# Kernel tuning notes

Measured on AMD Instinct MI355X. Metric: run time of the kernel, lower is better.

Reference implementation:

```python
import jax, jax.numpy as jnp
import numpy as np

EPS = 1e-6

def _ste(x, xq):
    return x + jax.lax.stop_gradient(xq - x)

def rmsnorm(x, w):
    return x * jax.lax.rsqrt(jnp.mean(x * x, axis=-1, keepdims=True) + EPS) * w

def act_quant(x):
    # per-token absmax int8 quantization (BitNet b1.58)
    s = 127.0 / jnp.clip(jnp.max(jnp.abs(x), axis=-1, keepdims=True), 1e-5)
    return _ste(x, jnp.clip(jnp.round(x * s), -128, 127) / s)

def w_quant(w):
    # per-tensor mean-absmax ternary quantization
    s = 1.0 / jnp.clip(jnp.mean(jnp.abs(w)), 1e-5)
    return _ste(w, jnp.clip(jnp.round(w * s), -1, 1) / s)

def bitlinear(x, w):
    return act_quant(x) @ w_quant(w).T

def snake_beta(x, log_a, log_b):
    a = jnp.exp(log_a)
    b = jnp.exp(log_b)
    s = jnp.sin(a * x)
    return x + (1.0 / (b + 1e-9)) * s * s

def ffn(x, nw, w1, la, lb, w2):
    h = bitlinear(rmsnorm(x, nw), w1)
    return bitlinear(snake_beta(h, la, lb), w2)

def mha(x, nw, ipw, ipb, opw, opb, num_heads):
    B, T, D = x.shape
    hd = D // num_heads
    xn = rmsnorm(x, nw)
    qkv = xn @ ipw.T + ipb  # [B,T,3D]
    q, k, v = jnp.split(qkv, 3, axis=-1)
    def heads(t):
        return t.reshape(B, T, num_heads, hd).transpose(0, 2, 1, 3)  # [B,H,T,hd]
    q, k, v = heads(q), heads(k), heads(v)
    scores = jnp.einsum('bhqd,bhkd->bhqk', q, k) / jnp.sqrt(jnp.asarray(hd, x.dtype))
    attn = jax.nn.softmax(scores, axis=-1)
    o = jnp.einsum('bhqk,bhkd->bhqd', attn, v)
    o = o.transpose(0, 2, 1, 3).reshape(B, T, D)
    return o @ opw.T + opb

def conv_branch(x, nw, pw1, dw, dwb, bg, bb, bm, bv, la, lb, pw2, K):
    B, T, D = x.shape
    h = rmsnorm(x, nw)
    h = bitlinear(h, pw1)  # [B,T,2D] (1x1 BitConv1d)
    a, g = jnp.split(h, 2, axis=-1)
    h = a * jax.nn.sigmoid(g)  # GLU over channels
    hc = h.transpose(0, 2, 1)  # [B,D,T]
    hc = jax.lax.conv_general_dilated(
        hc, dw, window_strides=(1,), padding=[(K // 2, K // 2)],
        feature_group_count=D, dimension_numbers=('NCH', 'OIH', 'NCH'))
    hc = hc + dwb[None, :, None]
    hc = (hc - bm[None, :, None]) * jax.lax.rsqrt(bv[None, :, None] + 1e-5) * bg[None, :, None] + bb[None, :, None]
    h = hc.transpose(0, 2, 1)  # [B,T,D]
    h = snake_beta(h, la, lb)
    return bitlinear(h, pw2)

def setup_inputs() -> dict:
    key = jax.random.key(0)
    B, T, D, H, K = 4, 2048, 512, 8, 31
    ks = jax.random.split(key, 16)
    n = lambda k, s: (jax.random.normal(k, s, jnp.float32) * 0.02)
    d = {
        'x': jax.random.normal(ks[0], (B, T, D), jnp.float32),
        'ff1_norm_w': jnp.ones((D,), jnp.float32),
        'ff1_w1': n(ks[1], (4 * D, D)), 'ff1_a': jnp.zeros((4 * D,), jnp.float32),
        'ff1_b': jnp.zeros((4 * D,), jnp.float32), 'ff1_w2': n(ks[2], (D, 4 * D)),
        'attn_norm_w': jnp.ones((D,), jnp.float32),
        'in_proj_w': n(ks[3], (3 * D, D)), 'in_proj_b': jnp.zeros((3 * D,), jnp.float32),
        'out_proj_w': n(ks[4], (D, D)), 'out_proj_b': jnp.zeros((D,), jnp.float32),
        'conv_norm_w': jnp.ones((D,), jnp.float32),
        'pw1_w': n(ks[5], (2 * D, D)),
        'dw_w': n(ks[6], (D, 1, K)), 'dw_b': jnp.zeros((D,), jnp.float32),
        'bn_g': jnp.ones((D,), jnp.float32), 'bn_b': jnp.zeros((D,), jnp.float32),
        'bn_m': jnp.zeros((D,), jnp.float32), 'bn_v': jnp.ones((D,), jnp.float32),
        'snake_a': jnp.zeros((D,), jnp.float32), 'snake_b': jnp.zeros((D,), jnp.float32),
        'pw2_w': n(ks[7], (D, D)),
        'ff2_norm_w': jnp.ones((D,), jnp.float32),
        'ff2_w1': n(ks[8], (4 * D, D)), 'ff2_a': jnp.zeros((4 * D,), jnp.float32),
        'ff2_b': jnp.zeros((4 * D,), jnp.float32), 'ff2_w2': n(ks[9], (D, 4 * D)),
        'final_norm_w': jnp.ones((D,), jnp.float32),
    }
    return d

def reference(x, ff1_norm_w, ff1_w1, ff1_a, ff1_b, ff1_w2, attn_norm_w, in_proj_w, in_proj_b, out_proj_w, out_proj_b, conv_norm_w, pw1_w, dw_w, dw_b, bn_g, bn_b, bn_m, bn_v, snake_a, snake_b, pw2_w, ff2_norm_w, ff2_w1, ff2_a, ff2_b, ff2_w2, final_norm_w):
    H, K = 8, 31
    x = x + 0.5 * ffn(x, ff1_norm_w, ff1_w1, ff1_a, ff1_b, ff1_w2)
    x = x + mha(x, attn_norm_w, in_proj_w, in_proj_b, out_proj_w, out_proj_b, H)
    x = x + conv_branch(x, conv_norm_w, pw1_w, dw_w, dw_b, bn_g, bn_b, bn_m, bn_v, snake_a, snake_b, pw2_w, K)
    x = x + 0.5 * ffn(x, ff2_norm_w, ff2_w1, ff2_a, ff2_b, ff2_w2)
    return rmsnorm(x, final_norm_w)
```

## Files before the change

kernel.cpp:

```cpp
#include <hip/hip_runtime.h>
#include <math.h>


typedef int   v4i __attribute__((ext_vector_type(4)));
typedef float v4f __attribute__((ext_vector_type(4)));
typedef float v16f __attribute__((ext_vector_type(16)));
typedef short v8s __attribute__((ext_vector_type(8)));
typedef unsigned short u16;

#define GLOAD_LDS(g, l) __builtin_amdgcn_global_load_lds( \
    (const __attribute__((address_space(1))) void*)(g),   \
    (__attribute__((address_space(3))) void*)(l), 16, 0, 0)

__device__ __forceinline__ float blk_sum256(float v, float* sm) {
#pragma unroll
  for (int m = 32; m; m >>= 1) v += __shfl_xor(v, m);
  int w = threadIdx.x >> 6;
  __syncthreads();
  if ((threadIdx.x & 63) == 0) sm[w] = v;
  __syncthreads();
  return sm[0] + sm[1] + sm[2] + sm[3];
}

__device__ __forceinline__ u16 f2bf(float f) {
  union { float f; unsigned u; } x;
  x.f = f;
  unsigned r = x.u + 0x7fffu + ((x.u >> 16) & 1u);
  return (u16)(r >> 16);
}

__device__ __forceinline__ float bf2f(u16 u) {
  union { unsigned u; float f; } x;
  x.u = ((unsigned)u) << 16;
  return x.f;
}

__device__ __forceinline__ void xcd_tiles(int& tx, int& ty) {
  int nx = gridDim.x;
  int flat = blockIdx.y * nx + blockIdx.x;
  int nwg = nx * gridDim.y;
  int cpx = nwg >> 3;
  int swz = (flat & 7) * cpx + (flat >> 3);
  ty = swz / nx;
  tx = swz - ty * nx;
}

__global__ __launch_bounds__(256) void wabs_stage1(
    const float* __restrict__ w0, const float* __restrict__ w1,
    const float* __restrict__ w2, const float* __restrict__ w3,
    const float* __restrict__ w4, const float* __restrict__ w5,
    float* __restrict__ part) {
  __shared__ float sm[4];
  const float* ws[6] = {w0, w1, w2, w3, w4, w5};
  const int ns[6] = {1048576, 1048576, 524288, 262144, 1048576, 1048576};
  int widx = blockIdx.x >> 6;
  int chunk = blockIdx.x & 63;
  const float* w = ws[widx];
  int n = ns[widx];
  float s = 0.f;
  for (int i = chunk * 256 + threadIdx.x; i < n; i += 64 * 256) s += fabsf(w[i]);
  s = blk_sum256(s, sm);
  if (threadIdx.x == 0) part[widx * 64 + chunk] = s;
}

__global__ __launch_bounds__(256) void wquant_all(
    const float* __restrict__ w0, const float* __restrict__ w1,
    const float* __restrict__ w2, const float* __restrict__ w3,
    const float* __restrict__ w4, const float* __restrict__ w5,
    const float* __restrict__ part, float* __restrict__ scales,
    signed char* __restrict__ out) {
  const float* ws[6] = {w0, w1, w2, w3, w4, w5};
  const int ns[6] = {1048576, 1048576, 524288, 262144, 1048576, 1048576};
  const int offs[6] = {0, 1048576, 2097152, 2621440, 2883584, 3932160};
  int widx = blockIdx.y;
  const float* w = ws[widx];
  int n = ns[widx];
  signed char* o = out + offs[widx];
  float ssum = 0.f;
#pragma unroll 8
  for (int i = 0; i < 64; ++i) ssum += part[widx * 64 + i];
  float wsc = fmaxf(ssum / (float)n, 1e-5f);
  if (blockIdx.x == 0 && threadIdx.x == 0) scales[widx] = wsc;
  float s = 1.0f / wsc;
  for (int i = blockIdx.x * 256 + threadIdx.x; i < n; i += 128 * 256)
    o[i] = (signed char)(int)fminf(fmaxf(rintf(w[i] * s), -1.f), 1.f);
}

__global__ __launch_bounds__(256) void wcvt_tabs(
    const float* __restrict__ ip, const float* __restrict__ op, u16* __restrict__ wb,
    const float* __restrict__ a1, const float* __restrict__ b1,
    const float* __restrict__ a2, const float* __restrict__ b2,
    float* __restrict__ tabs, const float* __restrict__ x, u16* __restrict__ xbf) {
  int bid = blockIdx.x;
  if (bid < 4096) {
    int i = bid * 256 + threadIdx.x;
    if (i < 786432) wb[i] = f2bf(ip[i]);
    else wb[i] = f2bf(op[i - 786432]);
  } else if (bid < 4104) {
    int i = (bid - 4096) * 256 + threadIdx.x;
    if (i < 2048) {
      tabs[i] = __expf(a1[i]);
      tabs[2048 + i] = 1.0f / (__expf(b1[i]) + 1e-9f);
      tabs[4096 + i] = __expf(a2[i]);
      tabs[6144 + i] = 1.0f / (__expf(b2[i]) + 1e-9f);
    }
  } else {
    size_t i = ((size_t)(bid - 4104) * 256 + threadIdx.x) * 8;
    float4 f0 = *(const float4*)(x + i);
    float4 f1 = *(const float4*)(x + i + 4);
    v8s o;
    o[0] = (short)f2bf(f0.x); o[1] = (short)f2bf(f0.y);
    o[2] = (short)f2bf(f0.z); o[3] = (short)f2bf(f0.w);
    o[4] = (short)f2bf(f1.x); o[5] = (short)f2bf(f1.y);
    o[6] = (short)f2bf(f1.z); o[7] = (short)f2bf(f1.w);
    *(v8s*)(xbf + i) = o;
  }
}

__global__ __launch_bounds__(256) void rmsnorm_wave(
    const u16* __restrict__ x, const float* __restrict__ w, int mode,
    float* __restrict__ outf, signed char* __restrict__ out8,
    u16* __restrict__ outb, float* __restrict__ dq) {
  const int tid = threadIdx.x;
  const int lane = tid & 63, wv = tid >> 6;
  const int row = blockIdx.x * 4 + wv;
  const int c0 = lane * 8;
  v8s xv = *(const v8s*)(x + (size_t)row * 512 + c0);
  float v[8];
  float ss = 0.f;
#pragma unroll
  for (int j = 0; j < 8; ++j) {
    v[j] = bf2f((u16)xv[j]);
    ss = fmaf(v[j], v[j], ss);
  }
#pragma unroll
  for (int m = 1; m < 64; m <<= 1) ss += __shfl_xor(ss, m);
  float sc = 1.0f / sqrtf(ss * (1.0f / 512.0f) + 1e-6f);
  float4 w0 = *(const float4*)(w + c0);
  float4 w1 = *(const float4*)(w + c0 + 4);
  float wv8[8] = {w0.x, w0.y, w0.z, w0.w, w1.x, w1.y, w1.z, w1.w};
  float y[8];
#pragma unroll
  for (int j = 0; j < 8; ++j) y[j] = v[j] * sc * wv8[j];
  if (mode == 0) {
    float* o = outf + (size_t)row * 512 + c0;
    *(float4*)o = make_float4(y[0], y[1], y[2], y[3]);
    *(float4*)(o + 4) = make_float4(y[4], y[5], y[6], y[7]);
  } else if (mode == 1) {
    float am = 0.f;
#pragma unroll
    for (int j = 0; j < 8; ++j) am = fmaxf(am, fabsf(y[j]));
#pragma unroll
    for (int m = 1; m < 64; m <<= 1) am = fmaxf(am, __shfl_xor(am, m));
    float amc = fmaxf(am, 1e-5f);
    float s = 127.0f / amc;
    unsigned long long pkt = 0;
#pragma unroll
    for (int j = 0; j < 8; ++j) {
      int q = (int)rintf(y[j] * s);
      pkt |= ((unsigned long long)(unsigned char)(signed char)q) << (8 * j);
    }
    *(unsigned long long*)(out8 + (size_t)row * 512 + c0) = pkt;
    if (lane == 0) dq[row] = amc * (1.0f / 127.0f);
  } else {
    v8s o;
#pragma unroll
    for (int j = 0; j < 8; ++j) o[j] = (short)f2bf(y[j]);
    *(v8s*)(outb + (size_t)row * 512 + c0) = o;
  }
}

__global__ __launch_bounds__(256) void snake_wave(
    const u16* __restrict__ h, const float* __restrict__ ta, const float* __restrict__ tb,
    signed char* __restrict__ out, float* __restrict__ dq) {
  const int tid = threadIdx.x;
  const int lane = tid & 63, wv = tid >> 6;
  const int row = blockIdx.x * 4 + wv;
  const u16* hr = h + (size_t)row * 2048;
  float vals[32];
  float am = 0.f;
#pragma unroll
  for (int g = 0; g < 4; ++g) {
    int c0 = g * 512 + lane * 8;
    v8s hv = *(const v8s*)(hr + c0);
    float4 ta0 = *(const float4*)(ta + c0);
    float4 ta1 = *(const float4*)(ta + c0 + 4);
    float4 tb0 = *(const float4*)(tb + c0);
    float4 tb1 = *(const float4*)(tb + c0 + 4);
    float sa[8] = {ta0.x, ta0.y, ta0.z, ta0.w, ta1.x, ta1.y, ta1.z, ta1.w};
    float sib[8] = {tb0.x, tb0.y, tb0.z, tb0.w, tb1.x, tb1.y, tb1.z, tb1.w};
#pragma unroll
    for (int j = 0; j < 8; ++j) {
      float v = bf2f((u16)hv[j]);
      float s = __sinf(sa[j] * v);
      v += s * s * sib[j];
      vals[g * 8 + j] = v;
      am = fmaxf(am, fabsf(v));
    }
  }
#pragma unroll
  for (int m = 1; m < 64; m <<= 1) am = fmaxf(am, __shfl_xor(am, m));
  float amc = fmaxf(am, 1e-5f);
  float s = 127.0f / amc;
#pragma unroll
  for (int g = 0; g < 4; ++g) {
    unsigned long long pkt = 0;
#pragma unroll
    for (int j = 0; j < 8; ++j) {
      int q = (int)rintf(vals[g * 8 + j] * s);
      pkt |= ((unsigned long long)(unsigned char)(signed char)q) << (8 * j);
    }
    *(unsigned long long*)(out + (size_t)row * 2048 + g * 512 + lane * 8) = pkt;
  }
  if (lane == 0) dq[row] = amc * (1.0f / 127.0f);
}

__global__ __launch_bounds__(256) void rowquant_wave(
    const u16* __restrict__ in, signed char* __restrict__ out, float* __restrict__ dq) {
  const int tid = threadIdx.x;
  const int lane = tid & 63, wv = tid >> 6;
  const int row = blockIdx.x * 4 + wv;
  const int c0 = lane * 8;
  v8s xv = *(const v8s*)(in + (size_t)row * 512 + c0);
  float v[8];
  float am = 0.f;
#pragma unroll
  for (int j = 0; j < 8; ++j) {
    v[j] = bf2f((u16)xv[j]);
    am = fmaxf(am, fabsf(v[j]));
  }
#pragma unroll
  for (int m = 1; m < 64; m <<= 1) am = fmaxf(am, __shfl_xor(am, m));
  float amc = fmaxf(am, 1e-5f);
  float s = 127.0f / amc;
  unsigned long long pkt = 0;
#pragma unroll
  for (int j = 0; j < 8; ++j) {
    int q = (int)rintf(v[j] * s);
    pkt |= ((unsigned long long)(unsigned char)(signed char)q) << (8 * j);
  }
  *(unsigned long long*)(out + (size_t)row * 512 + c0) = pkt;
  if (lane == 0) dq[row] = amc * (1.0f / 127.0f);
}

template <int BN, int OM>
__global__ __launch_bounds__(256) void gemm_i8_t(
    const signed char* __restrict__ A, const signed char* __restrict__ B,
    const float* __restrict__ wsp, const float* __restrict__ adq,
    const u16* __restrict__ resid, float rscale,
    u16* __restrict__ outb, int N, int K) {
  constexpr int JF = BN / 32;
  __shared__ signed char As[16384];
  __shared__ signed char Bs[BN * 128];
  const int tid = threadIdx.x;
  int txc, tyc;
  xcd_tiles(txc, tyc);
  const int m0 = tyc << 7;
  const int n0 = txc * BN;
  const int lane = tid & 63;
  const int wv = tid >> 6;
  const int wr = (wv >> 1) << 6, wc = (wv & 1) * (16 * JF);
  const int r15 = lane & 15, khi = lane >> 4;
  const int srow = tid >> 3;
  const int sslot = (tid & 7) ^ (srow & 7);
  const signed char* Ag = A + (size_t)(m0 + srow) * K + sslot * 16;
  const signed char* Bg = B + (size_t)(n0 + srow) * K + sslot * 16;
  const size_t row32 = (size_t)32 * K;

  int aoff[4][2], boff[JF][2];
#pragma unroll
  for (int i = 0; i < 4; ++i) {
    int r = wr + i * 16 + r15;
#pragma unroll
    for (int s = 0; s < 2; ++s)
      aoff[i][s] = r * 128 + (((s << 2) + khi) ^ (r & 7)) * 16;
  }
#pragma unroll
  for (int j = 0; j < JF; ++j) {
    int c = wc + j * 16 + r15;
#pragma unroll
    for (int s = 0; s < 2; ++s)
      boff[j][s] = c * 128 + (((s << 2) + khi) ^ (c & 7)) * 16;
  }
  v4i acc[4][JF] = {};
  for (int k0 = 0; k0 < K; k0 += 128) {
    __syncthreads();
#pragma unroll
    for (int c = 0; c < 4; ++c)
      GLOAD_LDS(Ag + c * row32 + k0, As + c * 4096 + tid * 16);
#pragma unroll
    for (int c = 0; c < BN / 32; ++c)
      GLOAD_LDS(Bg + c * row32 + k0, Bs + c * 4096 + tid * 16);
    __syncthreads();
    v4i a[4][2], b[JF][2];
#pragma unroll
    for (int i = 0; i < 4; ++i) {
      a[i][0] = *(const v4i*)(As + aoff[i][0]);
      a[i][1] = *(const v4i*)(As + aoff[i][1]);
    }
#pragma unroll
    for (int j = 0; j < JF; ++j) {
      b[j][0] = *(const v4i*)(Bs + boff[j][0]);
      b[j][1] = *(const v4i*)(Bs + boff[j][1]);
    }
#pragma unroll
    for (int i = 0; i < 4; ++i)
#pragma unroll
      for (int j = 0; j < JF; ++j) {
        acc[i][j] = __builtin_amdgcn_mfma_i32_16x16x64_i8(a[i][0], b[j][0], acc[i][j], 0, 0, 0);
        acc[i][j] = __builtin_amdgcn_mfma_i32_16x16x64_i8(a[i][1], b[j][1], acc[i][j], 0, 0, 0);
      }
  }
  const float wsc = *wsp;
#pragma unroll
  for (int i = 0; i < 4; ++i) {
    int rb = m0 + wr + i * 16 + (khi << 2);
    float dqv[4];
#pragma unroll
    for (int rr = 0; rr < 4; ++rr) dqv[rr] = adq[rb + rr] * wsc;
#pragma unroll
    for (int j = 0; j < JF; ++j) {
      int col = n0 + wc + j * 16 + r15;
#pragma unroll
      for (int rr = 0; rr < 4; ++rr) {
        size_t idx = (size_t)(rb + rr) * N + col;
        float v = (float)acc[i][j][rr] * dqv[rr];
        if constexpr (OM == 0) outb[idx] = f2bf(v);
        else outb[idx] = f2bf(fmaf(rscale, v, bf2f(resid[idx])));
      }
    }
  }
}

template <int BN, int OM>
__global__ __launch_bounds__(256) void gemm_bf16_t(
    const u16* __restrict__ A, const u16* __restrict__ B,
    const float* __restrict__ bias, const u16* __restrict__ resid,
    u16* __restrict__ outb, int N, int K) {
  constexpr int JF = BN / 32;
  __shared__ signed char As[8192];
  __shared__ signed char Bs[BN * 64];
  const int tid = threadIdx.x;
  int txc, tyc;
  xcd_tiles(txc, tyc);
  const int m0 = tyc << 7;
  const int n0 = txc * BN;
  const int lane = tid & 63;
  const int wv = tid >> 6;
  const int wr = (wv >> 1) << 6, wc = (wv & 1) * (16 * JF);
  const int r15 = lane & 15, khi = lane >> 4;
  const int srow = tid >> 2;
  const int sslot = (tid & 3) ^ ((srow >> 1) & 3);
  const int K2 = K * 2;
  const signed char* Ag = (const signed char*)A + (size_t)(m0 + srow) * K2 + sslot * 16;
  const signed char* Bg = (const signed char*)B + (size_t)(n0 + srow) * K2 + sslot * 16;
  const size_t half = (size_t)64 * K2;

  int aoff[4], boff[JF];
#pragma unroll
  for (int i = 0; i < 4; ++i) {
    int r = wr + i * 16 + r15;
    aoff[i] = r * 64 + ((khi ^ ((r >> 1) & 3)) << 4);
  }
#pragma unroll
  for (int j = 0; j < JF; ++j) {
    int c = wc + j * 16 + r15;
    boff[j] = c * 64 + ((khi ^ ((c >> 1) & 3)) << 4);
  }
  v4f acc[4][JF] = {};
  for (int kb = 0; kb < K2; kb += 64) {
    __syncthreads();
    GLOAD_LDS(Ag + kb, As + tid * 16);
    GLOAD_LDS(Ag + half + kb, As + 4096 + tid * 16);
    GLOAD_LDS(Bg + kb, Bs + tid * 16);
    if constexpr (BN == 128) GLOAD_LDS(Bg + half + kb, Bs + 4096 + tid * 16);
    __syncthreads();
    v8s a[4], b[JF];
#pragma unroll
    for (int i = 0; i < 4; ++i) a[i] = *(const v8s*)(As + aoff[i]);
#pragma unroll
    for (int j = 0; j < JF; ++j) b[j] = *(const v8s*)(Bs + boff[j]);
#pragma unroll
    for (int i = 0; i < 4; ++i)
#pragma unroll
      for (int j = 0; j < JF; ++j)
        acc[i][j] = __builtin_amdgcn_mfma_f32_16x16x32_bf16(a[i], b[j], acc[i][j], 0, 0, 0);
  }
#pragma unroll
  for (int i = 0; i < 4; ++i) {
    int rb = m0 + wr + i * 16 + (khi << 2);
#pragma unroll
    for (int j = 0; j < JF; ++j) {
      int col = n0 + wc + j * 16 + r15;
      float bv = bias[col];
#pragma unroll
      for (int rr = 0; rr < 4; ++rr) {
        size_t idx = (size_t)(rb + rr) * N + col;
        float v = acc[i][j][rr] + bv;
        if constexpr (OM == 0) outb[idx] = f2bf(v);
        else outb[idx] = f2bf(bf2f(resid[idx]) + v);
      }
    }
  }
}

__global__ __launch_bounds__(256) void kvqpack(
    const u16* __restrict__ qkv, u16* __restrict__ kvqp) {
  __shared__ u16 Lv[32 * 72];
  const int tid = threadIdx.x;
  const int tile = blockIdx.x;
  const int bh = blockIdx.y;
  const int b = bh >> 3, h = bh & 7;
  u16* outb = kvqp + ((size_t)(bh * 64 + tile)) * 6144;
  const int lane = tid & 63, f = tid >> 6;
  const int l31 = lane & 31, hi = lane >> 5;

  {
    int r = tid >> 3, c = (tid & 7) << 3;
    const u16* src = qkv + (size_t)(b * 2048 + tile * 32 + r) * 1536 + 1024 + h * 64 + c;
    *(v8s*)(&Lv[r * 72 + c]) = *(const v8s*)src;
  }
  {
    const u16* src = qkv + (size_t)(b * 2048 + tile * 32 + l31) * 1536 + h * 64 + f * 16 + hi * 8;
    *(v8s*)(outb + (size_t)(8 + f) * 512 + lane * 8) = *(const v8s*)src;
  }
  {
    const u16* src = qkv + (size_t)(b * 2048 + tile * 32 + l31) * 1536 + 512 + h * 64 + f * 16 + hi * 8;
    *(v8s*)(outb + (size_t)f * 512 + lane * 8) = *(const v8s*)src;
  }
  __syncthreads();
  {
    int d = ((f >> 1) << 5) + l31;
    int tbase = ((f & 1) << 4) + hi * 8;
    v8s v;
#pragma unroll
    for (int j = 0; j < 8; ++j) v[j] = (short)Lv[(tbase + j) * 72 + d];
    *(v8s*)(outb + (size_t)(4 + f) * 512 + lane * 8) = v;
  }
}

__global__ __launch_bounds__(256) void attn32(
    const u16* __restrict__ kvqp, u16* __restrict__ opart, float* __restrict__ ml) {
  __shared__ u16 KV[2][4096];
  const int tid = threadIdx.x;
  const int lane = tid & 63;
  const int wv = tid >> 6;
  const int l31 = lane & 31;
  const int hi = lane >> 5;
  const int bh = blockIdx.y;
  const int z = blockIdx.z;
  const int b = bh >> 3, h = bh & 7;
  const int qt = blockIdx.x * 4 + wv;
  const int q0 = qt << 5;
  const float C = 0.18033688011112042f;

  v8s qf[4];
  {
    const u16* qb = kvqp + ((size_t)(bh * 64 + qt)) * 6144 + lane * 8;
#pragma unroll
    for (int ks = 0; ks < 4; ++ks) qf[ks] = *(const v8s*)(qb + (8 + ks) * 512);
  }
  v16f o0 = {}, o1 = {};
  float m_run = -INFINITY, l_run = 0.f;

  const u16* tb = kvqp + ((size_t)(bh * 64 + z * 16)) * 6144;

  GLOAD_LDS(tb + tid * 8, &KV[0][tid * 8]);
  GLOAD_LDS(tb + 2048 + tid * 8, &KV[0][2048 + tid * 8]);
  __syncthreads();

  int cur = 0;
  for (int t = 0; t < 16; ++t) {
    if (t < 15) {
      const u16* nb = tb + (size_t)(t + 1) * 6144;
      GLOAD_LDS(nb + tid * 8, &KV[cur ^ 1][tid * 8]);
      GLOAD_LDS(nb + 2048 + tid * 8, &KV[cur ^ 1][2048 + tid * 8]);
    }
    v8s kf[4], vf[4];
#pragma unroll
    for (int ks = 0; ks < 4; ++ks) kf[ks] = *(const v8s*)(&KV[cur][ks * 512 + lane * 8]);
#pragma unroll
    for (int j = 0; j < 4; ++j) vf[j] = *(const v8s*)(&KV[cur][2048 + j * 512 + lane * 8]);

    __builtin_amdgcn_s_setprio(1);
    v16f sacc = {};
#pragma unroll
    for (int ks = 0; ks < 4; ++ks)
      sacc = __builtin_amdgcn_mfma_f32_32x32x16_bf16(kf[ks], qf[ks], sacc, 0, 0, 0);
    __builtin_amdgcn_s_setprio(0);

    float s[16];
#pragma unroll
    for (int r = 0; r < 16; ++r) s[r] = sacc[r];
    float m0v = fmaxf(fmaxf(s[0], s[1]), s[2]);
    float m1v = fmaxf(fmaxf(s[3], s[4]), s[5]);
    float m2v = fmaxf(fmaxf(s[6], s[7]), s[8]);
    float m3v = fmaxf(fmaxf(s[9], s[10]), s[11]);
    float m4v = fmaxf(fmaxf(s[12], s[13]), s[14]);
    float t0v = fmaxf(fmaxf(m0v, m1v), m2v);
    float t1v = fmaxf(fmaxf(m3v, m4v), s[15]);
    float mx = fmaxf(t0v, t1v);
    {
      float tsw = mx;
      asm("v_permlane32_swap_b32 %0, %1" : "+v"(tsw), "+v"(mx));
      mx = fmaxf(mx, tsw);
    }
    if (__any((mx - m_run) * C > 8.0f)) {
      float mn = fmaxf(m_run, mx);
      float corr = exp2f((m_run - mn) * C);
      m_run = mn;
      l_run *= corr;
#pragma unroll
      for (int r = 0; r < 16; ++r) { o0[r] *= corr; o1[r] *= corr; }
    }
    float mnC = m_run * C;
#pragma unroll
    for (int r = 0; r < 16; ++r) s[r] = exp2f(fmaf(s[r], C, -mnC));

    {
      float a0 = (s[0] + s[1]) + (s[2] + s[3]);
      float a1 = (s[4] + s[5]) + (s[6] + s[7]);
      float a2 = (s[8] + s[9]) + (s[10] + s[11]);
      float a3 = (s[12] + s[13]) + (s[14] + s[15]);
      float ls = (a0 + a1) + (a2 + a3);
      float tsw = ls;
      asm("v_permlane32_swap_b32 %0, %1" : "+v"(tsw), "+v"(ls));
      l_run += ls + tsw;
    }

    unsigned pk[8];
#pragma unroll
    for (int g = 0; g < 8; ++g) {
      unsigned u;
      asm("v_cvt_pk_bf16_f32 %0, %1, %2" : "=v"(u) : "v"(s[2 * g]), "v"(s[2 * g + 1]));
      pk[g] = u;
    }
    asm("v_permlane32_swap_b32 %0, %1" : "+v"(pk[2]), "+v"(pk[0]));
    asm("v_permlane32_swap_b32 %0, %1" : "+v"(pk[3]), "+v"(pk[1]));
    asm("v_permlane32_swap_b32 %0, %1" : "+v"(pk[6]), "+v"(pk[4]));
    asm("v_permlane32_swap_b32 %0, %1" : "+v"(pk[7]), "+v"(pk[5]));
    v4i w0, w1;
    w0[0] = pk[0]; w0[1] = pk[1]; w0[2] = pk[2]; w0[3] = pk[3];
    w1[0] = pk[4]; w1[1] = pk[5]; w1[2] = pk[6]; w1[3] = pk[7];
    v8s pf0 = *(v8s*)&w0;
    v8s pf1 = *(v8s*)&w1;

    __builtin_amdgcn_s_setprio(1);
    o0 = __builtin_amdgcn_mfma_f32_32x32x16_bf16(vf[0], pf0, o0, 0, 0, 0);
    o0 = __builtin_amdgcn_mfma_f32_32x32x16_bf16(vf[1], pf1, o0, 0, 0, 0);
    o1 = __builtin_amdgcn_mfma_f32_32x32x16_bf16(vf[2], pf0, o1, 0, 0, 0);
    o1 = __builtin_amdgcn_mfma_f32_32x32x16_bf16(vf[3], pf1, o1, 0, 0, 0);
    __builtin_amdgcn_s_setprio(0);

    __syncthreads();
    cur ^= 1;
  }

  float inv = 1.0f / l_run;
  u16* orow = opart + (size_t)z * 4194304 + (size_t)(b * 2048 + q0 + l31) * 512 + h * 64;
#pragma unroll
  for (int dt = 0; dt < 2; ++dt) {
#pragma unroll
    for (int g = 0; g < 8; ++g) {
      int d = dt * 32 + ((2 * g) & 3) + 8 * (g >> 1) + 4 * hi;
      float a = (dt ? o1[2 * g] : o0[2 * g]) * inv;
      float bv = (dt ? o1[2 * g + 1] : o0[2 * g + 1]) * inv;
      unsigned u;
      asm("v_cvt_pk_bf16_f32 %0, %1, %2" : "=v"(u) : "v"(a), "v"(bv));
      *(unsigned*)(orow + d) = u;
    }
  }
  if (hi == 0) {
    size_t mi = ((size_t)(z * 8192 + b * 2048 + q0 + l31) * 8 + h) * 2;
    ml[mi] = m_run;
    ml[mi + 1] = l_run;
  }
}

__global__ __launch_bounds__(256) void attn_merge(
    const u16* __restrict__ opart, const float* __restrict__ ml,
    u16* __restrict__ attno) {
  __shared__ float wsm[4][8];
  const int r = blockIdx.x, tid = threadIdx.x;
  if (tid < 8) {
    const float C = 0.18033688011112042f;
    float m[4], l[4];
#pragma unroll
    for (int z = 0; z < 4; ++z) {
      size_t i = ((size_t)(z * 8192 + r) * 8 + tid) * 2;
      m[z] = ml[i];
      l[z] = ml[i + 1];
    }
    float M = fmaxf(fmaxf(m[0], m[1]), fmaxf(m[2], m[3]));
    float a[4], sum = 0.f;
#pragma unroll
    for (int z = 0; z < 4; ++z) {
      a[z] = exp2f((m[z] - M) * C) * l[z];
      sum += a[z];
    }
    float inv = 1.0f / sum;
#pragma unroll
    for (int z = 0; z < 4; ++z) wsm[z][tid] = a[z] * inv;
  }
  __syncthreads();
  int c = tid * 2;
  int hh = c >> 6;
  float x0 = 0.f, x1 = 0.f;
#pragma unroll
  for (int z = 0; z < 4; ++z) {
    unsigned p = *(const unsigned*)(opart + (size_t)z * 4194304 + (size_t)r * 512 + c);
    float w = wsm[z][hh];
    x0 = fmaf(bf2f((u16)p), w, x0);
    x1 = fmaf(bf2f((u16)(p >> 16)), w, x1);
  }
  unsigned u;
  asm("v_cvt_pk_bf16_f32 %0, %1, %2" : "=v"(u) : "v"(x0), "v"(x1));
  *(unsigned*)(attno + (size_t)r * 512 + c) = u;
}

__global__ __launch_bounds__(256) void dwconv_fused(
    const u16* __restrict__ g3, const float* __restrict__ dww,
    const float* __restrict__ dwb, const float* __restrict__ bng,
    const float* __restrict__ bnb, const float* __restrict__ bnm,
    const float* __restrict__ bnv, const float* __restrict__ la,
    const float* __restrict__ lb, u16* __restrict__ outp) {
  __shared__ float IN[160 * 64];
  __shared__ float WT[1984];
  __shared__ float PRM[4][64];
  const int tid = threadIdx.x;
  const int cg = blockIdx.x << 6;
  const int t0 = blockIdx.y << 7;
  const int bb = blockIdx.z;

  if (tid < 64) {
    int c = cg + tid;
    float sc = bng[c] / sqrtf(bnv[c] + 1e-5f);
    PRM[0][tid] = sc;
    PRM[1][tid] = (dwb[c] - bnm[c]) * sc + bnb[c];
    PRM[2][tid] = __expf(la[c]);
    PRM[3][tid] = 1.0f / (__expf(lb[c]) + 1e-9f);
  }
  for (int i = tid; i < 1984; i += 256) WT[i] = dww[cg * 31 + i];

#pragma unroll
  for (int p = 0; p < 5; ++p) {
    int r = p * 32 + (tid >> 3);
    int t = t0 - 16 + r;
    int c8 = (tid & 7) << 3;
    float4 lo = make_float4(0.f, 0.f, 0.f, 0.f);
    float4 hv = make_float4(0.f, 0.f, 0.f, 0.f);
    if (t >= 0 && t < 2048) {
      const u16* rp = g3 + ((size_t)(bb * 2048 + t)) * 1024 + cg + c8;
      v8s a8 = *(const v8s*)rp;
      v8s g8 = *(const v8s*)(rp + 512);
      float va[8];
#pragma unroll
      for (int j = 0; j < 8; ++j) {
        float fa = bf2f((u16)a8[j]);
        float fg = bf2f((u16)g8[j]);
        va[j] = fa / (1.f + __expf(-fg));
      }
      lo = make_float4(va[0], va[1], va[2], va[3]);
      hv = make_float4(va[4], va[5], va[6], va[7]);
    }
    *(float4*)&IN[r * 64 + c8] = lo;
    *(float4*)&IN[r * 64 + c8 + 4] = hv;
  }
  __syncthreads();

  const int ch = tid & 63;
  const int tg = tid >> 6;
  const float sc = PRM[0][ch], sh = PRM[1][ch], sa = PRM[2][ch], sib = PRM[3][ch];
  float w[31];
#pragma unroll
  for (int k = 0; k < 31; ++k) w[k] = WT[ch * 31 + k];

  for (int pass = 0; pass < 4; ++pass) {
    int tl = pass * 32 + tg * 8;
    float x[38];
#pragma unroll
    for (int i = 0; i < 38; ++i) x[i] = IN[(tl + 1 + i) * 64 + ch];
    float acc[8] = {0.f, 0.f, 0.f, 0.f, 0.f, 0.f, 0.f, 0.f};
#pragma unroll
    for (int k = 0; k < 31; ++k)
#pragma unroll
      for (int j = 0; j < 8; ++j) acc[j] = fmaf(x[k + j], w[k], acc[j]);
#pragma unroll
    for (int j = 0; j < 8; ++j) {
      float v = acc[j] * sc + sh;
      float s = __sinf(sa * v);
      v += s * s * sib;
      outp[((size_t)(bb * 2048 + t0 + tl + j)) * 512 + cg + ch] = f2bf(v);
    }
  }
}

extern "C" void kernel_launch(void* const* d_in, const int* in_sizes, int n_in,
                              void* d_out, int out_size, void* d_ws, size_t ws_size,
                              hipStream_t stream) {
  const float* x_in = (const float*)d_in[0];
  const float* ff1_norm_w = (const float*)d_in[1];
  const float* ff1_w1 = (const float*)d_in[2];
  const float* ff1_a = (const float*)d_in[3];
  const float* ff1_b = (const float*)d_in[4];
  const float* ff1_w2 = (const float*)d_in[5];
  const float* attn_norm_w = (const float*)d_in[6];
  const float* in_proj_w = (const float*)d_in[7];
  const float* in_proj_b = (const float*)d_in[8];
  const float* out_proj_w = (const float*)d_in[9];
  const float* out_proj_b = (const float*)d_in[10];
  const float* conv_norm_w = (const float*)d_in[11];
  const float* pw1_w = (const float*)d_in[12];
  const float* dw_w = (const float*)d_in[13];
  const float* dw_b = (const float*)d_in[14];
  const float* bn_g = (const float*)d_in[15];
  const float* bn_b = (const float*)d_in[16];
  const float* bn_m = (const float*)d_in[17];
  const float* bn_v = (const float*)d_in[18];
  const float* snake_a = (const float*)d_in[19];
  const float* snake_b = (const float*)d_in[20];
  const float* pw2_w = (const float*)d_in[21];
  const float* ff2_norm_w = (const float*)d_in[22];
  const float* ff2_w1 = (const float*)d_in[23];
  const float* ff2_a = (const float*)d_in[24];
  const float* ff2_b = (const float*)d_in[25];
  const float* ff2_w2 = (const float*)d_in[26];
  const float* final_norm_w = (const float*)d_in[27];
  float* out = (float*)d_out;

  char* ws = (char*)d_ws;
  u16* x_bf = (u16*)(ws + 0);
  u16* x_cur = (u16*)(ws + 8388608);
  u16* qkv = (u16*)(ws + 16777216);
  u16* kvqp = (u16*)(ws + 41943040);
  u16* opart = (u16*)(ws + 67108864);
  u16* attno = (u16*)(ws + 100663296);
  float* ml = (float*)(ws + 109051904);
  u16* h_b = (u16*)(ws + 16777216);
  u16* g3b = (u16*)(ws + 16777216);
  u16* convout = (u16*)(ws + 50331648);
  signed char* a8a = (signed char*)(ws + 83886080);
  signed char* a8b = (signed char*)(ws + 88080384);
  u16* xnb = (u16*)(ws + 104857600);
  signed char* wq = (signed char*)(ws + 113246208);
  signed char* wq_w1 = wq;
  signed char* wq_w2 = wq + 1048576;
  signed char* wq_p1 = wq + 2097152;
  signed char* wq_p2 = wq + 2621440;
  signed char* wq_f21 = wq + 2883584;
  signed char* wq_f22 = wq + 3932160;
  u16* wb = (u16*)(ws + 118226944);
  u16* wb_ip = wb;
  u16* wb_op = wb + 786432;
  float* scales = (float*)(ws + 120324096);
  float* partials = (float*)(ws + 120324352);
  float* ascale = (float*)(ws + 120325888);
  float* tabs = (float*)(ws + 120358912);

  wabs_stage1<<<384, 256, 0, stream>>>(ff1_w1, ff1_w2, pw1_w, pw2_w, ff2_w1, ff2_w2, partials);
  wquant_all<<<dim3(128, 6), 256, 0, stream>>>(ff1_w1, ff1_w2, pw1_w, pw2_w, ff2_w1, ff2_w2,
                                               partials, scales, wq);
  wcvt_tabs<<<6152, 256, 0, stream>>>(in_proj_w, out_proj_w, wb, ff1_a, ff1_b, ff2_a, ff2_b,
                                      tabs, x_in, x_bf);

  rmsnorm_wave<<<2048, 256, 0, stream>>>(x_bf, ff1_norm_w, 1, nullptr, a8a, nullptr, ascale);
  gemm_i8_t<128, 0><<<dim3(16, 64), 256, 0, stream>>>(
      a8a, wq_w1, scales + 0, ascale, nullptr, 1.0f, h_b, 2048, 512);
  snake_wave<<<2048, 256, 0, stream>>>(h_b, tabs, tabs + 2048, a8b, ascale);
  gemm_i8_t<64, 1><<<dim3(8, 64), 256, 0, stream>>>(
      a8b, wq_w2, scales + 1, ascale, x_bf, 0.5f, x_cur, 512, 2048);

  rmsnorm_wave<<<2048, 256, 0, stream>>>(x_cur, attn_norm_w, 2, nullptr, nullptr, xnb, nullptr);
  gemm_bf16_t<128, 0><<<dim3(12, 64), 256, 0, stream>>>(
      xnb, wb_ip, in_proj_b, nullptr, qkv, 1536, 512);
  kvqpack<<<dim3(64, 32), 256, 0, stream>>>(qkv, kvqp);
  attn32<<<dim3(16, 32, 4), 256, 0, stream>>>(kvqp, opart, ml);
  attn_merge<<<8192, 256, 0, stream>>>(opart, ml, attno);
  gemm_bf16_t<64, 1><<<dim3(8, 64), 256, 0, stream>>>(
      attno, wb_op, out_proj_b, x_cur, x_cur, 512, 512);

  rmsnorm_wave<<<2048, 256, 0, stream>>>(x_cur, conv_norm_w, 1, nullptr, a8a, nullptr, ascale);
  gemm_i8_t<128, 0><<<dim3(8, 64), 256, 0, stream>>>(
      a8a, wq_p1, scales + 2, ascale, nullptr, 1.0f, g3b, 1024, 512);
  dwconv_fused<<<dim3(8, 16, 4), 256, 0, stream>>>(g3b, dw_w, dw_b, bn_g, bn_b, bn_m, bn_v,
                                                   snake_a, snake_b, convout);
  rowquant_wave<<<2048, 256, 0, stream>>>(convout, a8a, ascale);
  gemm_i8_t<64, 1><<<dim3(8, 64), 256, 0, stream>>>(
      a8a, wq_p2, scales + 3, ascale, x_cur, 1.0f, x_cur, 512, 512);

  rmsnorm_wave<<<2048, 256, 0, stream>>>(x_cur, ff2_norm_w, 1, nullptr, a8a, nullptr, ascale);
  gemm_i8_t<128, 0><<<dim3(16, 64), 256, 0, stream>>>(
      a8a, wq_f21, scales + 4, ascale, nullptr, 1.0f, h_b, 2048, 512);
  snake_wave<<<2048, 256, 0, stream>>>(h_b, tabs + 4096, tabs + 6144, a8b, ascale);
  gemm_i8_t<64, 1><<<dim3(8, 64), 256, 0, stream>>>(
      a8b, wq_f22, scales + 5, ascale, x_cur, 0.5f, x_cur, 512, 2048);

  rmsnorm_wave<<<2048, 256, 0, stream>>>(x_cur, final_norm_w, 0, out, nullptr, nullptr, nullptr);
}
```

Before: 308.5 us.

## Fuse input bf16 cast into first rmsnorm, vectorize weight cast, halve attention splits

Moves the fp32-to-bf16 conversion of the input into a new rmsnorm kernel that reads fp32 directly, writes both the bf16 residual copy and the int8 quantized activations, and saves one pass over x. The projection-weight cast now handles four elements per thread with float4 loads, so the launch has far fewer blocks. Attention key splits drop from four to two, with 32 key tiles per block and a cheaper two-way merge. This halves the attention grid, which may reduce parallelism while cutting merge traffic. A stray declaration `unsigned short4_t{}` is left in the weight-cast kernel.

```diff
diff --git a/kernel.cpp b/kernel.cpp
--- a/kernel.cpp
+++ b/kernel.cpp
@@ -90,31 +90,75 @@
     const float* __restrict__ ip, const float* __restrict__ op, u16* __restrict__ wb,
     const float* __restrict__ a1, const float* __restrict__ b1,
     const float* __restrict__ a2, const float* __restrict__ b2,
-    float* __restrict__ tabs, const float* __restrict__ x, u16* __restrict__ xbf) {
+    float* __restrict__ tabs) {
   int bid = blockIdx.x;
-  if (bid < 4096) {
+  if (bid < 1024) {
     int i = bid * 256 + threadIdx.x;
-    if (i < 786432) wb[i] = f2bf(ip[i]);
-    else wb[i] = f2bf(op[i - 786432]);
-  } else if (bid < 4104) {
-    int i = (bid - 4096) * 256 + threadIdx.x;
+    float4 f;
+    if (i < 196608) f = *(const float4*)(ip + (size_t)i * 4);
+    else f = *(const float4*)(op + (size_t)(i - 196608) * 4);
+    unsigned short4_t{};
+    u16* dst = wb + (size_t)i * 4;
+    dst[0] = f2bf(f.x); dst[1] = f2bf(f.y); dst[2] = f2bf(f.z); dst[3] = f2bf(f.w);
+  } else {
+    int i = (bid - 1024) * 256 + threadIdx.x;
     if (i < 2048) {
       tabs[i] = __expf(a1[i]);
       tabs[2048 + i] = 1.0f / (__expf(b1[i]) + 1e-9f);
       tabs[4096 + i] = __expf(a2[i]);
       tabs[6144 + i] = 1.0f / (__expf(b2[i]) + 1e-9f);
     }
-  } else {
-    size_t i = ((size_t)(bid - 4104) * 256 + threadIdx.x) * 8;
-    float4 f0 = *(const float4*)(x + i);
-    float4 f1 = *(const float4*)(x + i + 4);
-    v8s o;
-    o[0] = (short)f2bf(f0.x); o[1] = (short)f2bf(f0.y);
-    o[2] = (short)f2bf(f0.z); o[3] = (short)f2bf(f0.w);
-    o[4] = (short)f2bf(f1.x); o[5] = (short)f2bf(f1.y);
-    o[6] = (short)f2bf(f1.z); o[7] = (short)f2bf(f1.w);
-    *(v8s*)(xbf + i) = o;
-  }
+  }
+}
+
+__global__ __launch_bounds__(256) void rmsnorm_f32x(
+    const float* __restrict__ x, const float* __restrict__ w,
+    signed char* __restrict__ out8, u16* __restrict__ xbf,
+    float* __restrict__ dq) {
+  const int tid = threadIdx.x;
+  const int lane = tid & 63, wv = tid >> 6;
+  const int row = blockIdx.x * 4 + wv;
+  const int c0 = lane * 8;
+  const float* xr = x + (size_t)row * 512 + c0;
+  float4 f0 = *(const float4*)xr;
+  float4 f1 = *(const float4*)(xr + 4);
+  float fin[8] = {f0.x, f0.y, f0.z, f0.w, f1.x, f1.y, f1.z, f1.w};
+  v8s xb;
+  float v[8];
+  float ss = 0.f;
+#pragma unroll
+  for (int j = 0; j < 8; ++j) {
+    u16 b = f2bf(fin[j]);
+    xb[j] = (short)b;
+    v[j] = bf2f(b);
+    ss = fmaf(v[j], v[j], ss);
+  }
+  *(v8s*)(xbf + (size_t)row * 512 + c0) = xb;
+#pragma unroll
+  for (int m = 1; m < 64; m <<= 1) ss += __shfl_xor(ss, m);
+  float sc = 1.0f / sqrtf(ss * (1.0f / 512.0f) + 1e-6f);
+  float4 w0 = *(const float4*)(w + c0);
+  float4 w1 = *(const float4*)(w + c0 + 4);
+  float wv8[8] = {w0.x, w0.y, w0.z, w0.w, w1.x, w1.y, w1.z, w1.w};
+  float y[8];
+  float am = 0.f;
+#pragma unroll
+  for (int j = 0; j < 8; ++j) {
+    y[j] = v[j] * sc * wv8[j];
+    am = fmaxf(am, fabsf(y[j]));
+  }
+#pragma unroll
+  for (int m = 1; m < 64; m <<= 1) am = fmaxf(am, __shfl_xor(am, m));
+  float amc = fmaxf(am, 1e-5f);
+  float s = 127.0f / amc;
+  unsigned long long pkt = 0;
+#pragma unroll
+  for (int j = 0; j < 8; ++j) {
+    int q = (int)rintf(y[j] * s);
+    pkt |= ((unsigned long long)(unsigned char)(signed char)q) << (8 * j);
+  }
+  *(unsigned long long*)(out8 + (size_t)row * 512 + c0) = pkt;
+  if (lane == 0) dq[row] = amc * (1.0f / 127.0f);
 }
 
 __global__ __launch_bounds__(256) void rmsnorm_wave(
@@ -463,15 +507,15 @@
   v16f o0 = {}, o1 = {};
   float m_run = -INFINITY, l_run = 0.f;
 
-  const u16* tb = kvqp + ((size_t)(bh * 64 + z * 16)) * 6144;
+  const u16* tb = kvqp + ((size_t)(bh * 64 + z * 32)) * 6144;
 
   GLOAD_LDS(tb + tid * 8, &KV[0][tid * 8]);
   GLOAD_LDS(tb + 2048 + tid * 8, &KV[0][2048 + tid * 8]);
   __syncthreads();
 
   int cur = 0;
-  for (int t = 0; t < 16; ++t) {
-    if (t < 15) {
+  for (int t = 0; t < 32; ++t) {
+    if (t < 31) {
       const u16* nb = tb + (size_t)(t + 1) * 6144;
       GLOAD_LDS(nb + tid * 8, &KV[cur ^ 1][tid * 8]);
       GLOAD_LDS(nb + 2048 + tid * 8, &KV[cur ^ 1][2048 + tid * 8]);
@@ -580,34 +624,30 @@
 __global__ __launch_bounds__(256) void attn_merge(
     const u16* __restrict__ opart, const float* __restrict__ ml,
     u16* __restrict__ attno) {
-  __shared__ float wsm[4][8];
+  __shared__ float wsm[2][8];
   const int r = blockIdx.x, tid = threadIdx.x;
   if (tid < 8) {
     const float C = 0.18033688011112042f;
-    float m[4], l[4];
-#pragma unroll
-    for (int z = 0; z < 4; ++z) {
+    float m[2], l[2];
+#pragma unroll
+    for (int z = 0; z < 2; ++z) {
       size_t i = ((size_t)(z * 8192 + r) * 8 + tid) * 2;
       m[z] = ml[i];
       l[z] = ml[i + 1];
     }
-    float M = fmaxf(fmaxf(m[0], m[1]), fmaxf(m[2], m[3]));
-    float a[4], sum = 0.f;
-#pragma unroll
-    for (int z = 0; z < 4; ++z) {
-      a[z] = exp2f((m[z] - M) * C) * l[z];
-      sum += a[z];
-    }
-    float inv = 1.0f / sum;
-#pragma unroll
-    for (int z = 0; z < 4; ++z) wsm[z][tid] = a[z] * inv;
+    float M = fmaxf(m[0], m[1]);
+    float a0 = exp2f((m[0] - M) * C) * l[0];
+    float a1 = exp2f((m[1] - M) * C) * l[1];
+    float inv = 1.0f / (a0 + a1);
+    wsm[0][tid] = a0 * inv;
+    wsm[1][tid] = a1 * inv;
   }
   __syncthreads();
   int c = tid * 2;
   int hh = c >> 6;
   float x0 = 0.f, x1 = 0.f;
 #pragma unroll
-  for (int z = 0; z < 4; ++z) {
+  for (int z = 0; z < 2; ++z) {
     unsigned p = *(const unsigned*)(opart + (size_t)z * 4194304 + (size_t)r * 512 + c);
     float w = wsm[z][hh];
     x0 = fmaf(bf2f((u16)p), w, x0);
@@ -760,10 +800,10 @@
   wabs_stage1<<<384, 256, 0, stream>>>(ff1_w1, ff1_w2, pw1_w, pw2_w, ff2_w1, ff2_w2, partials);
   wquant_all<<<dim3(128, 6), 256, 0, stream>>>(ff1_w1, ff1_w2, pw1_w, pw2_w, ff2_w1, ff2_w2,
                                                partials, scales, wq);
-  wcvt_tabs<<<6152, 256, 0, stream>>>(in_proj_w, out_proj_w, wb, ff1_a, ff1_b, ff2_a, ff2_b,
-                                      tabs, x_in, x_bf);
-
-  rmsnorm_wave<<<2048, 256, 0, stream>>>(x_bf, ff1_norm_w, 1, nullptr, a8a, nullptr, ascale);
+  wcvt_tabs<<<1032, 256, 0, stream>>>(in_proj_w, out_proj_w, wb, ff1_a, ff1_b, ff2_a, ff2_b,
+                                      tabs);
+
+  rmsnorm_f32x<<<2048, 256, 0, stream>>>(x_in, ff1_norm_w, a8a, x_bf, ascale);
   gemm_i8_t<128, 0><<<dim3(16, 64), 256, 0, stream>>>(
       a8a, wq_w1, scales + 0, ascale, nullptr, 1.0f, h_b, 2048, 512);
   snake_wave<<<2048, 256, 0, stream>>>(h_b, tabs, tabs + 2048, a8b, ascale);
@@ -774,7 +814,7 @@
   gemm_bf16_t<128, 0><<<dim3(12, 64), 256, 0, stream>>>(
       xnb, wb_ip, in_proj_b, nullptr, qkv, 1536, 512);
   kvqpack<<<dim3(64, 32), 256, 0, stream>>>(qkv, kvqp);
-  attn32<<<dim3(16, 32, 4), 256, 0, stream>>>(kvqp, opart, ml);
+  attn32<<<dim3(16, 32, 2), 256, 0, stream>>>(kvqp, opart, ml);
   attn_merge<<<8192, 256, 0, stream>>>(opart, ml, attno);
   gemm_bf16_t<64, 1><<<dim3(8, 64), 256, 0, stream>>>(
       attno, wb_op, out_proj_b, x_cur, x_cur, 512, 512);
```

After: 300.6 us. 2.6% less time.
